# Kernel tuning notes

Measured on AMD Instinct MI355X. Metric: run time of the kernel, lower is better.

The kernel has to match this reference:

```python
import jax, jax.numpy as jnp
import numpy as np

B, D, O = 65536, 512, 64   # batch, input_size, output_size
E, T, K = 8, 2, 2          # num_experts, n_task, top-k
H1, H2 = 64, 32            # expert_hidden_layers (hardcoded in Expert)
LOSS_COEF = 0.01
EPS = 1e-10


def setup_inputs() -> dict:
    key = jax.random.key(0)
    ks = jax.random.split(key, 8)
    f32 = jnp.float32
    def rn(k, shape, scale):
        return jax.random.normal(k, shape, f32) * scale
    return {
        "x": jax.random.normal(ks[0], (B, D), f32),
        # gating params (one per task); init random so top-k routing is nontrivial
        "w_gates": rn(ks[1], (T, D, E), 0.02),
        "b_gates": jnp.zeros((T, E), f32),
        # per-expert MLP params, stacked over the expert axis
        "W1": rn(ks[2], (E, D, H1), 1.0 / np.sqrt(D)),
        "b1": jnp.zeros((E, H1), f32),
        "W2": rn(ks[3], (E, H1, H2), 1.0 / np.sqrt(H1)),
        "b2": jnp.zeros((E, H2), f32),
        "W3": rn(ks[4], (E, H2, O), 1.0 / np.sqrt(H2)),
        "b3": jnp.zeros((E, O), f32),
    }


def _cv_squared(v):
    # torch .var() default is unbiased (ddof=1)
    return jnp.var(v, ddof=1) / (jnp.mean(v) ** 2 + EPS)


def reference(x, w_gates, b_gates, W1, b1, W2, b2, W3, b3):
    # --- noisy_top_k_gating in eval mode (train=False): clean logits, top-k softmax ---
    logits = jnp.einsum("bd,tde->tbe", x, w_gates) + b_gates[:, None, :]  # [T,B,E]
    top_v, top_i = jax.lax.top_k(logits, K)                                # [T,B,K]
    top_g = jax.nn.softmax(top_v, axis=-1)                                 # [T,B,K]
    # scatter top-k gate values back to dense [T,B,E] (zeros elsewhere)
    gates = jnp.sum(jax.nn.one_hot(top_i, E, dtype=top_g.dtype) * top_g[..., None], axis=2)

    # --- experts: each token through each expert MLP (gates zero out non-selected,
    #     mathematically identical to dispatch/combine) ---
    h = jax.nn.relu(jnp.einsum("bd,edh->ebh", x, W1) + b1[:, None, :])     # [E,B,H1]
    h = jax.nn.relu(jnp.einsum("ebh,eho->ebo", h, W2) + b2[:, None, :])    # [E,B,H2]
    expert_out = jax.nn.relu(jnp.einsum("ebh,eho->ebo", h, W3) + b3[:, None, :])  # [E,B,O]

    # weighted combine per task
    y = jnp.einsum("tbe,ebo->tbo", gates, expert_out)                       # [T,B,O]

    # --- load balancing loss ---
    importance = gates.sum(axis=1)                          # [T,E]
    load = (gates > 0).sum(axis=1).astype(jnp.float32)      # [T,E]
    loss = LOSS_COEF * (jax.vmap(_cv_squared)(importance) + jax.vmap(_cv_squared)(load)).sum()
    return y, loss
```

## Files before the change

kernel.cpp:

```cpp
#include <hip/hip_runtime.h>


typedef short bfrag __attribute__((ext_vector_type(8)));
typedef float facc  __attribute__((ext_vector_type(4)));

#define MFMA16(a, b, c) __builtin_amdgcn_mfma_f32_16x16x32_bf16((a), (b), (c), 0, 0, 0)

__device__ __forceinline__ unsigned short bfbits(float f) {
  unsigned int u = __builtin_bit_cast(unsigned int, f);
  u += 0x7FFFu + ((u >> 16) & 1u);
  return (unsigned short)(u >> 16);
}
__device__ __forceinline__ unsigned pack2(float a, float b) {
  return (unsigned)bfbits(a) | ((unsigned)bfbits(b) << 16);
}
__device__ __forceinline__ float bf2f(unsigned short s) {
  unsigned int u = ((unsigned int)s) << 16;
  return __builtin_bit_cast(float, u);
}

#define G_OFF   65536
#define R_OFF   70656
#define A_OFF   72704
#define SM_SIZE 72832

__global__ __launch_bounds__(512, 4) void moe_fused(
    const float* __restrict__ x,
    const float* __restrict__ b_gates,
    const float* __restrict__ wgt,
    const float* __restrict__ b1,
    const float* __restrict__ b2,
    const float* __restrict__ b3,
    const bfrag* __restrict__ w1f,
    const bfrag* __restrict__ w2f,
    const bfrag* __restrict__ w3f,
    float* __restrict__ gacc_out,
    float* __restrict__ y)
{
  __shared__ alignas(16) char smem[SM_SIZE];
  const int tid = threadIdx.x;
  const int wave = tid >> 6, lane = tid & 63;
  const int q = lane & 15, g = lane >> 4;
  const int e = wave;
  const unsigned cb = (unsigned)e * 8192u;

  if (tid < 32) ((float*)(smem + A_OFF))[tid] = 0.f;

  const float* src = x + (size_t)blockIdx.x * 64 * 512 + lane * 512 + wave * 64;
  float4 fr[16];
  #pragma unroll
  for (int j = 0; j < 16; ++j) fr[j] = ((const float4*)src)[j];

  {
    int wu = __builtin_amdgcn_readfirstlane(wave);
    const float* wbase = wgt + wu * 64;
    float* pp = (float*)(smem + wave * 4096 + lane * 64);
    #pragma unroll
    for (int te = 0; te < 16; ++te) {
      const float* wrow = wbase + te * 512;
      float a0 = 0.f, a1 = 0.f, a2 = 0.f, a3 = 0.f;
      #pragma unroll
      for (int j = 0; j < 16; ++j) {
        a0 = fmaf(fr[j].x, wrow[j * 4 + 0], a0);
        a1 = fmaf(fr[j].y, wrow[j * 4 + 1], a1);
        a2 = fmaf(fr[j].z, wrow[j * 4 + 2], a2);
        a3 = fmaf(fr[j].w, wrow[j * 4 + 3], a3);
      }
      pp[(te + lane) & 15] = (a0 + a1) + (a2 + a3);
    }
  }
  __syncthreads();

  #pragma unroll
  for (int i0 = 0; i0 < 2; ++i0) {
    int i = i0 * 512 + tid;
    int tok = i >> 4, te = i & 15;
    const float* pb = (const float*)smem + tok * 16 + ((te + tok) & 15);
    float s = 0.f;
    #pragma unroll
    for (int w2 = 0; w2 < 8; ++w2) s += pb[w2 * 1024];
    ((float*)(smem + G_OFF))[tok * 20 + te] = s + b_gates[te];
  }
  __syncthreads();

  #pragma unroll
  for (int p = 0; p < 8; ++p) {
    uint4 v;
    v.x = pack2(fr[2 * p].x, fr[2 * p].y);
    v.y = pack2(fr[2 * p].z, fr[2 * p].w);
    v.z = pack2(fr[2 * p + 1].x, fr[2 * p + 1].y);
    v.w = pack2(fr[2 * p + 1].z, fr[2 * p + 1].w);
    unsigned byte = ((unsigned)(lane * 1024 + wave * 128 + p * 16)) ^ ((unsigned)(lane & 7) << 4);
    *(uint4*)(smem + byte) = v;
  }

  if (tid < 128) {
    int tok = tid >> 1, task = tid & 1;
    const float* Gr = (const float*)(smem + G_OFF) + tok * 20 + task * 8;
    float l[8];
    #pragma unroll
    for (int ee = 0; ee < 8; ++ee) l[ee] = Gr[ee];
    float v1 = l[0]; int e1 = 0;
    #pragma unroll
    for (int ee = 1; ee < 8; ++ee) { if (l[ee] > v1) { v1 = l[ee]; e1 = ee; } }
    float v2 = -3.4e38f; int e2 = 0;
    #pragma unroll
    for (int ee = 0; ee < 8; ++ee) {
      if (ee != e1 && l[ee] > v2) { v2 = l[ee]; e2 = ee; }
    }
    float g1 = 1.f / (1.f + __expf(v2 - v1));
    float g2 = 1.f - g1;
    float4 rec;
    rec.x = g1; rec.y = g2;
    rec.z = __int_as_float(e1); rec.w = __int_as_float(e2);
    ((float4*)(smem + R_OFF))[tok * 2 + task] = rec;
    float* lacc = (float*)(smem + A_OFF);
    atomicAdd(lacc + task * 8 + e1, g1);
    atomicAdd(lacc + task * 8 + e2, g2);
    atomicAdd(lacc + 16 + task * 8 + e1, 1.f);
    atomicAdd(lacc + 16 + task * 8 + e2, 1.f);
  }
  __syncthreads();

  facc acc[4][4];
  #pragma unroll
  for (int m = 0; m < 4; ++m)
    #pragma unroll
    for (int n = 0; n < 4; ++n) acc[m][n] = (facc)0.f;

  const bfrag* w1e = w1f + e * 4096 + lane;
  bfrag Bc[4], Bn[4];
  #pragma unroll
  for (int n = 0; n < 4; ++n) Bc[n] = w1e[n * 64];
  #pragma unroll
  for (int ks = 0; ks < 16; ++ks) {
    if (ks < 15) {
      #pragma unroll
      for (int n = 0; n < 4; ++n) Bn[n] = w1e[(ks + 1) * 256 + n * 64];
    }
    #pragma unroll
    for (int m = 0; m < 4; ++m) {
      unsigned ba = ((unsigned)((m * 16 + q) * 1024 + ks * 64 + g * 16)) ^ ((unsigned)(q & 7) << 4);
      bfrag A = *(const bfrag*)(smem + ba);
      #pragma unroll
      for (int n = 0; n < 4; ++n) acc[m][n] = MFMA16(A, Bc[n], acc[m][n]);
    }
    if (ks < 15) {
      #pragma unroll
      for (int n = 0; n < 4; ++n) Bc[n] = Bn[n];
    }
  }

  bfrag W2r[4];
  #pragma unroll
  for (int i = 0; i < 4; ++i) W2r[i] = w2f[e * 256 + i * 64 + lane];
  float b2v0 = b2[e * 32 + q];
  float b2v1 = b2[e * 32 + 16 + q];
  __syncthreads();

  {
    float bv[4];
    #pragma unroll
    for (int n = 0; n < 4; ++n) bv[n] = b1[e * 64 + n * 16 + q];
    #pragma unroll
    for (int m = 0; m < 4; ++m) {
      #pragma unroll
      for (int j = 0; j < 4; ++j) {
        float v0 = fmaxf(acc[m][0][j] + bv[0], 0.f);
        float v1 = fmaxf(acc[m][1][j] + bv[1], 0.f);
        float v2 = fmaxf(acc[m][2][j] + bv[2], 0.f);
        float v3 = fmaxf(acc[m][3][j] + bv[3], 0.f);
        int rr = m * 16 + g * 4 + j;
        unsigned byte = cb + (((unsigned)(rr * 128 + q * 8)) ^ ((unsigned)(rr & 7) << 4));
        uint2 p; p.x = pack2(v0, v1); p.y = pack2(v2, v3);
        *(uint2*)(smem + byte) = p;
      }
    }
  }

  {
    facc a2[4][2];
    #pragma unroll
    for (int m = 0; m < 4; ++m) { a2[m][0] = (facc)0.f; a2[m][1] = (facc)0.f; }
    #pragma unroll
    for (int ks = 0; ks < 2; ++ks) {
      #pragma unroll
      for (int m = 0; m < 4; ++m) {
        unsigned ba = cb + (((unsigned)((m * 16 + q) * 128 + ks * 64 + g * 16)) ^ ((unsigned)(q & 7) << 4));
        bfrag A = *(const bfrag*)(smem + ba);
        #pragma unroll
        for (int n = 0; n < 2; ++n) a2[m][n] = MFMA16(A, W2r[ks * 2 + n], a2[m][n]);
      }
    }
    bfrag W3r[4];
    #pragma unroll
    for (int n = 0; n < 4; ++n) W3r[n] = w3f[e * 256 + n * 64 + lane];
    float b3v[4];
    #pragma unroll
    for (int n = 0; n < 4; ++n) b3v[n] = b3[e * 64 + n * 16 + q];

    #pragma unroll
    for (int m = 0; m < 4; ++m) {
      #pragma unroll
      for (int j = 0; j < 4; ++j) {
        float v0 = fmaxf(a2[m][0][j] + b2v0, 0.f);
        float v1 = fmaxf(a2[m][1][j] + b2v1, 0.f);
        int rr = m * 16 + g * 4 + j;
        unsigned byte = cb + (((unsigned)(rr * 64 + q * 4)) ^ ((unsigned)(rr & 7) << 4));
        *(unsigned int*)(smem + byte) = pack2(v0, v1);
      }
    }

    facc a3[4][4];
    #pragma unroll
    for (int m = 0; m < 4; ++m)
      #pragma unroll
      for (int n = 0; n < 4; ++n) a3[m][n] = (facc)0.f;
    #pragma unroll
    for (int m = 0; m < 4; ++m) {
      unsigned ba = cb + (((unsigned)((m * 16 + q) * 64 + g * 16)) ^ ((unsigned)(q & 7) << 4));
      bfrag A = *(const bfrag*)(smem + ba);
      #pragma unroll
      for (int n = 0; n < 4; ++n) a3[m][n] = MFMA16(A, W3r[n], a3[m][n]);
    }
    #pragma unroll
    for (int m = 0; m < 4; ++m) {
      #pragma unroll
      for (int j = 0; j < 4; ++j) {
        float v0 = fmaxf(a3[m][0][j] + b3v[0], 0.f);
        float v1 = fmaxf(a3[m][1][j] + b3v[1], 0.f);
        float v2 = fmaxf(a3[m][2][j] + b3v[2], 0.f);
        float v3 = fmaxf(a3[m][3][j] + b3v[3], 0.f);
        int rr = m * 16 + g * 4 + j;
        unsigned byte = cb + (((unsigned)(rr * 128 + q * 8)) ^ ((unsigned)(rr & 7) << 4));
        uint2 p; p.x = pack2(v0, v1); p.y = pack2(v2, v3);
        *(uint2*)(smem + byte) = p;
      }
    }
  }
  __syncthreads();

  {
    int tsub = tid >> 4, u = tid & 15;
    const float4* recs = (const float4*)(smem + R_OFF);
    #pragma unroll
    for (int half = 0; half < 2; ++half) {
      int tok = tsub + half * 32;
      size_t trow = (size_t)blockIdx.x * 64 + tok;
      unsigned obyte = ((unsigned)(tok * 128 + u * 8)) ^ ((unsigned)(tok & 7) << 4);
      #pragma unroll
      for (int tt = 0; tt < 2; ++tt) {
        float4 rec = recs[tok * 2 + tt];
        float g1 = rec.x, g2 = rec.y;
        int e1 = __float_as_int(rec.z), e2 = __float_as_int(rec.w);
        uint2 o1 = *(const uint2*)(smem + e1 * 8192 + obyte);
        uint2 o2 = *(const uint2*)(smem + e2 * 8192 + obyte);
        unsigned short s1[4] = { (unsigned short)o1.x, (unsigned short)(o1.x >> 16),
                                 (unsigned short)o1.y, (unsigned short)(o1.y >> 16) };
        unsigned short s2[4] = { (unsigned short)o2.x, (unsigned short)(o2.x >> 16),
                                 (unsigned short)o2.y, (unsigned short)(o2.y >> 16) };
        float* yt = y + (size_t)tt * 4194304 + trow * 64;
        #pragma unroll
        for (int w = 0; w < 4; ++w) {
          yt[w * 16 + u] = g1 * bf2f(s1[w]) + g2 * bf2f(s2[w]);
        }
      }
    }
  }
  if (tid < 32) atomicAdd(gacc_out + tid, ((float*)(smem + A_OFF))[tid]);
  __syncthreads();

  if (tid == 0) {
    unsigned* cnt = (unsigned*)(gacc_out + 32);
    unsigned old = atomicAdd(cnt, 1u);
    if (old == gridDim.x - 1) {
      float loss = 0.f;
      #pragma unroll
      for (int a = 0; a < 4; ++a) {
        float v[8]; float mm = 0.f;
        #pragma unroll
        for (int i = 0; i < 8; ++i) {
          v[i] = __hip_atomic_load(gacc_out + a * 8 + i, __ATOMIC_RELAXED,
                                   __HIP_MEMORY_SCOPE_AGENT);
          mm += v[i];
        }
        mm *= 0.125f;
        float var = 0.f;
        #pragma unroll
        for (int i = 0; i < 8; ++i) { float d = v[i] - mm; var += d * d; }
        loss += (var * (1.f / 7.f)) / (mm * mm + 1e-10f);
      }
      y[8388608] = 0.01f * loss;
    }
  }
}

__global__ __launch_bounds__(256) void moe_prep(
    const float* __restrict__ W1, const float* __restrict__ W2,
    const float* __restrict__ W3, const float* __restrict__ wg,
    bfrag* __restrict__ w1f, bfrag* __restrict__ w2f,
    bfrag* __restrict__ w3f, float* __restrict__ wgt,
    float* __restrict__ gacc)
{
  int tid = blockIdx.x * 256 + threadIdx.x;
  bfrag o;
  if (tid < 32768) {
    int lane = tid & 63, nt = (tid >> 6) & 3, ks = (tid >> 8) & 15, e = tid >> 12;
    int q = lane & 15, g = lane >> 4;
    int hcol = nt * 16 + q;
    #pragma unroll
    for (int j = 0; j < 8; ++j) {
      int k = ks * 32 + g * 8 + j;
      o[j] = (short)bfbits(W1[((e * 512 + k) * 64) + hcol]);
    }
    w1f[tid] = o;
  } else if (tid < 34816) {
    int idx = tid - 32768;
    int lane = idx & 63, nt = (idx >> 6) & 1, ks = (idx >> 7) & 1, e = idx >> 8;
    int q = lane & 15, g = lane >> 4;
    int n = nt * 16 + q;
    #pragma unroll
    for (int j = 0; j < 8; ++j) {
      int s = ks * 32 + g * 8 + j;
      int hh = (s & 3) * 16 + (s >> 2);
      o[j] = (short)bfbits(W2[(e * 64 + hh) * 32 + n]);
    }
    w2f[idx] = o;
  } else if (tid < 36864) {
    int idx = tid - 34816;
    int lane = idx & 63, nt = (idx >> 6) & 3, e = idx >> 8;
    int q = lane & 15, g = lane >> 4;
    int ocol = nt * 16 + q;
    #pragma unroll
    for (int j = 0; j < 8; ++j) {
      int s = g * 8 + j;
      int hh = (s & 1) * 16 + (s >> 1);
      o[j] = (short)bfbits(W3[(e * 32 + hh) * 64 + ocol]);
    }
    w3f[idx] = o;
  } else if (tid < 45056) {
    int idx = tid - 36864;
    int te = idx >> 9, k = idx & 511;
    wgt[idx] = wg[(((te >> 3) * 512) + k) * 8 + (te & 7)];
  } else if (tid < 45089) {
    gacc[tid - 45056] = 0.f;
  }
}

extern "C" void kernel_launch(void* const* d_in, const int* in_sizes, int n_in,
                              void* d_out, int out_size, void* d_ws, size_t ws_size,
                              hipStream_t stream) {
  const float* x  = (const float*)d_in[0];
  const float* wg = (const float*)d_in[1];
  const float* bg = (const float*)d_in[2];
  const float* W1 = (const float*)d_in[3];
  const float* b1 = (const float*)d_in[4];
  const float* W2 = (const float*)d_in[5];
  const float* b2 = (const float*)d_in[6];
  const float* W3 = (const float*)d_in[7];
  const float* b3 = (const float*)d_in[8];
  float* y = (float*)d_out;

  char* ws = (char*)d_ws;
  float*  gacc = (float*)ws;
  bfrag*  w1f  = (bfrag*)(ws + 256);
  bfrag*  w2f  = (bfrag*)(ws + 524544);
  bfrag*  w3f  = (bfrag*)(ws + 557312);
  float*  wgt  = (float*)(ws + 590080);

  moe_prep<<<177, 256, 0, stream>>>(W1, W2, W3, wg, w1f, w2f, w3f, wgt, gacc);
  moe_fused<<<1024, 512, 0, stream>>>(x, bg, wgt, b1, b2, b3, w1f, w2f, w3f, gacc, y);
}
```

Before: 87.75 us.

## Halve tokens per block to 32 to cut LDS and registers for higher occupancy

Each block now processes 32 tokens instead of 64, with two lanes per token splitting the K range in the gating dot products. Shared memory roughly halves, per-wave accumulators shrink, and the grid doubles with launch bounds raised to 6 blocks per CU, all to raise occupancy and latency hiding. The W1 fragment double-buffer prefetch is removed. In exchange, W1, W2 and W3 fragments are re-read from global or L2 twice as often per token, the global atomics double, and the gate partial-sum reduction now spans 16 partials.

```diff
diff --git a/kernel.cpp b/kernel.cpp
--- a/kernel.cpp
+++ b/kernel.cpp
@@ -19,12 +19,12 @@
   return __builtin_bit_cast(float, u);
 }
 
-#define G_OFF   65536
-#define R_OFF   70656
-#define A_OFF   72704
-#define SM_SIZE 72832
-
-__global__ __launch_bounds__(512, 4) void moe_fused(
+#define G_OFF   32768
+#define R_OFF   34944
+#define A_OFF   35968
+#define SM_SIZE 36096
+
+__global__ __launch_bounds__(512, 6) void moe_fused(
     const float* __restrict__ x,
     const float* __restrict__ b_gates,
     const float* __restrict__ wgt,
@@ -42,61 +42,67 @@
   const int wave = tid >> 6, lane = tid & 63;
   const int q = lane & 15, g = lane >> 4;
   const int e = wave;
-  const unsigned cb = (unsigned)e * 8192u;
+  const unsigned cb = (unsigned)e * 4096u;
+  const int tok = lane & 31;
+  const int kh  = lane >> 5;
 
   if (tid < 32) ((float*)(smem + A_OFF))[tid] = 0.f;
 
-  const float* src = x + (size_t)blockIdx.x * 64 * 512 + lane * 512 + wave * 64;
-  float4 fr[16];
-  #pragma unroll
-  for (int j = 0; j < 16; ++j) fr[j] = ((const float4*)src)[j];
+  const float* src = x + (size_t)blockIdx.x * 32 * 512 + tok * 512 + wave * 64 + kh * 32;
+  float4 fr[8];
+  #pragma unroll
+  for (int j = 0; j < 8; ++j) fr[j] = ((const float4*)src)[j];
 
   {
     int wu = __builtin_amdgcn_readfirstlane(wave);
     const float* wbase = wgt + wu * 64;
-    float* pp = (float*)(smem + wave * 4096 + lane * 64);
+    float* pp = (float*)smem + ((wave * 2 + kh) * 32 + tok) * 16;
     #pragma unroll
     for (int te = 0; te < 16; ++te) {
       const float* wrow = wbase + te * 512;
       float a0 = 0.f, a1 = 0.f, a2 = 0.f, a3 = 0.f;
       #pragma unroll
-      for (int j = 0; j < 16; ++j) {
-        a0 = fmaf(fr[j].x, wrow[j * 4 + 0], a0);
-        a1 = fmaf(fr[j].y, wrow[j * 4 + 1], a1);
-        a2 = fmaf(fr[j].z, wrow[j * 4 + 2], a2);
-        a3 = fmaf(fr[j].w, wrow[j * 4 + 3], a3);
-      }
-      pp[(te + lane) & 15] = (a0 + a1) + (a2 + a3);
-    }
-  }
-  __syncthreads();
-
-  #pragma unroll
-  for (int i0 = 0; i0 < 2; ++i0) {
-    int i = i0 * 512 + tid;
-    int tok = i >> 4, te = i & 15;
-    const float* pb = (const float*)smem + tok * 16 + ((te + tok) & 15);
+      for (int j = 0; j < 8; ++j) {
+        float4 lo = *(const float4*)(wrow + j * 4);
+        float4 hi = *(const float4*)(wrow + 32 + j * 4);
+        float wx = kh ? hi.x : lo.x;
+        float wy = kh ? hi.y : lo.y;
+        float wz = kh ? hi.z : lo.z;
+        float ww = kh ? hi.w : lo.w;
+        a0 = fmaf(fr[j].x, wx, a0);
+        a1 = fmaf(fr[j].y, wy, a1);
+        a2 = fmaf(fr[j].z, wz, a2);
+        a3 = fmaf(fr[j].w, ww, a3);
+      }
+      pp[(te + (tok >> 1)) & 15] = (a0 + a1) + (a2 + a3);
+    }
+  }
+  __syncthreads();
+
+  {
+    int tk = tid >> 4, te = tid & 15;
+    const float* pb = (const float*)smem + tk * 16 + ((te + (tk >> 1)) & 15);
     float s = 0.f;
     #pragma unroll
-    for (int w2 = 0; w2 < 8; ++w2) s += pb[w2 * 1024];
-    ((float*)(smem + G_OFF))[tok * 20 + te] = s + b_gates[te];
-  }
-  __syncthreads();
-
-  #pragma unroll
-  for (int p = 0; p < 8; ++p) {
+    for (int c = 0; c < 16; ++c) s += pb[c * 512];
+    ((float*)(smem + G_OFF))[tk * 17 + te] = s + b_gates[te];
+  }
+  __syncthreads();
+
+  #pragma unroll
+  for (int p = 0; p < 4; ++p) {
     uint4 v;
     v.x = pack2(fr[2 * p].x, fr[2 * p].y);
     v.y = pack2(fr[2 * p].z, fr[2 * p].w);
     v.z = pack2(fr[2 * p + 1].x, fr[2 * p + 1].y);
     v.w = pack2(fr[2 * p + 1].z, fr[2 * p + 1].w);
-    unsigned byte = ((unsigned)(lane * 1024 + wave * 128 + p * 16)) ^ ((unsigned)(lane & 7) << 4);
+    unsigned byte = ((unsigned)(tok * 1024 + wave * 128 + kh * 64 + p * 16)) ^ ((unsigned)(tok & 7) << 4);
     *(uint4*)(smem + byte) = v;
   }
 
-  if (tid < 128) {
-    int tok = tid >> 1, task = tid & 1;
-    const float* Gr = (const float*)(smem + G_OFF) + tok * 20 + task * 8;
+  if (tid < 64) {
+    int ttok = tid >> 1, task = tid & 1;
+    const float* Gr = (const float*)(smem + G_OFF) + ttok * 17 + task * 8;
     float l[8];
     #pragma unroll
     for (int ee = 0; ee < 8; ++ee) l[ee] = Gr[ee];
@@ -113,7 +119,7 @@
     float4 rec;
     rec.x = g1; rec.y = g2;
     rec.z = __int_as_float(e1); rec.w = __int_as_float(e2);
-    ((float4*)(smem + R_OFF))[tok * 2 + task] = rec;
+    ((float4*)(smem + R_OFF))[ttok * 2 + task] = rec;
     float* lacc = (float*)(smem + A_OFF);
     atomicAdd(lacc + task * 8 + e1, g1);
     atomicAdd(lacc + task * 8 + e2, g2);
@@ -122,32 +128,27 @@
   }
   __syncthreads();
 
-  facc acc[4][4];
-  #pragma unroll
-  for (int m = 0; m < 4; ++m)
+  facc acc[2][4];
+  #pragma unroll
+  for (int m = 0; m < 2; ++m)
     #pragma unroll
     for (int n = 0; n < 4; ++n) acc[m][n] = (facc)0.f;
 
   const bfrag* w1e = w1f + e * 4096 + lane;
-  bfrag Bc[4], Bn[4];
-  #pragma unroll
-  for (int n = 0; n < 4; ++n) Bc[n] = w1e[n * 64];
   #pragma unroll
   for (int ks = 0; ks < 16; ++ks) {
-    if (ks < 15) {
-      #pragma unroll
-      for (int n = 0; n < 4; ++n) Bn[n] = w1e[(ks + 1) * 256 + n * 64];
-    }
-    #pragma unroll
-    for (int m = 0; m < 4; ++m) {
+    bfrag B0 = w1e[ks * 256];
+    bfrag B1 = w1e[ks * 256 + 64];
+    bfrag B2 = w1e[ks * 256 + 128];
+    bfrag B3 = w1e[ks * 256 + 192];
+    #pragma unroll
+    for (int m = 0; m < 2; ++m) {
       unsigned ba = ((unsigned)((m * 16 + q) * 1024 + ks * 64 + g * 16)) ^ ((unsigned)(q & 7) << 4);
       bfrag A = *(const bfrag*)(smem + ba);
-      #pragma unroll
-      for (int n = 0; n < 4; ++n) acc[m][n] = MFMA16(A, Bc[n], acc[m][n]);
-    }
-    if (ks < 15) {
-      #pragma unroll
-      for (int n = 0; n < 4; ++n) Bc[n] = Bn[n];
+      acc[m][0] = MFMA16(A, B0, acc[m][0]);
+      acc[m][1] = MFMA16(A, B1, acc[m][1]);
+      acc[m][2] = MFMA16(A, B2, acc[m][2]);
+      acc[m][3] = MFMA16(A, B3, acc[m][3]);
     }
   }
 
@@ -163,7 +164,7 @@
     #pragma unroll
     for (int n = 0; n < 4; ++n) bv[n] = b1[e * 64 + n * 16 + q];
     #pragma unroll
-    for (int m = 0; m < 4; ++m) {
+    for (int m = 0; m < 2; ++m) {
       #pragma unroll
       for (int j = 0; j < 4; ++j) {
         float v0 = fmaxf(acc[m][0][j] + bv[0], 0.f);
@@ -172,24 +173,24 @@
         float v3 = fmaxf(acc[m][3][j] + bv[3], 0.f);
         int rr = m * 16 + g * 4 + j;
         unsigned byte = cb + (((unsigned)(rr * 128 + q * 8)) ^ ((unsigned)(rr & 7) << 4));
-        uint2 p; p.x = pack2(v0, v1); p.y = pack2(v2, v3);
-        *(uint2*)(smem + byte) = p;
-      }
-    }
-  }
-
-  {
-    facc a2[4][2];
-    #pragma unroll
-    for (int m = 0; m < 4; ++m) { a2[m][0] = (facc)0.f; a2[m][1] = (facc)0.f; }
+        uint2 pk; pk.x = pack2(v0, v1); pk.y = pack2(v2, v3);
+        *(uint2*)(smem + byte) = pk;
+      }
+    }
+  }
+
+  {
+    facc a2[2][2];
+    #pragma unroll
+    for (int m = 0; m < 2; ++m) { a2[m][0] = (facc)0.f; a2[m][1] = (facc)0.f; }
     #pragma unroll
     for (int ks = 0; ks < 2; ++ks) {
       #pragma unroll
-      for (int m = 0; m < 4; ++m) {
+      for (int m = 0; m < 2; ++m) {
         unsigned ba = cb + (((unsigned)((m * 16 + q) * 128 + ks * 64 + g * 16)) ^ ((unsigned)(q & 7) << 4));
         bfrag A = *(const bfrag*)(smem + ba);
-        #pragma unroll
-        for (int n = 0; n < 2; ++n) a2[m][n] = MFMA16(A, W2r[ks * 2 + n], a2[m][n]);
+        a2[m][0] = MFMA16(A, W2r[ks * 2], a2[m][0]);
+        a2[m][1] = MFMA16(A, W2r[ks * 2 + 1], a2[m][1]);
       }
     }
     bfrag W3r[4];
@@ -200,7 +201,7 @@
     for (int n = 0; n < 4; ++n) b3v[n] = b3[e * 64 + n * 16 + q];
 
     #pragma unroll
-    for (int m = 0; m < 4; ++m) {
+    for (int m = 0; m < 2; ++m) {
       #pragma unroll
       for (int j = 0; j < 4; ++j) {
         float v0 = fmaxf(a2[m][0][j] + b2v0, 0.f);
@@ -211,20 +212,20 @@
       }
     }
 
-    facc a3[4][4];
-    #pragma unroll
-    for (int m = 0; m < 4; ++m)
+    facc a3[2][4];
+    #pragma unroll
+    for (int m = 0; m < 2; ++m)
       #pragma unroll
       for (int n = 0; n < 4; ++n) a3[m][n] = (facc)0.f;
     #pragma unroll
-    for (int m = 0; m < 4; ++m) {
+    for (int m = 0; m < 2; ++m) {
       unsigned ba = cb + (((unsigned)((m * 16 + q) * 64 + g * 16)) ^ ((unsigned)(q & 7) << 4));
       bfrag A = *(const bfrag*)(smem + ba);
       #pragma unroll
       for (int n = 0; n < 4; ++n) a3[m][n] = MFMA16(A, W3r[n], a3[m][n]);
     }
     #pragma unroll
-    for (int m = 0; m < 4; ++m) {
+    for (int m = 0; m < 2; ++m) {
       #pragma unroll
       for (int j = 0; j < 4; ++j) {
         float v0 = fmaxf(a3[m][0][j] + b3v[0], 0.f);
@@ -233,37 +234,33 @@
         float v3 = fmaxf(a3[m][3][j] + b3v[3], 0.f);
         int rr = m * 16 + g * 4 + j;
         unsigned byte = cb + (((unsigned)(rr * 128 + q * 8)) ^ ((unsigned)(rr & 7) << 4));
-        uint2 p; p.x = pack2(v0, v1); p.y = pack2(v2, v3);
-        *(uint2*)(smem + byte) = p;
-      }
-    }
-  }
-  __syncthreads();
-
-  {
-    int tsub = tid >> 4, u = tid & 15;
+        uint2 pk; pk.x = pack2(v0, v1); pk.y = pack2(v2, v3);
+        *(uint2*)(smem + byte) = pk;
+      }
+    }
+  }
+  __syncthreads();
+
+  {
+    int ct = tid >> 4, u = tid & 15;
+    size_t trow = (size_t)blockIdx.x * 32 + ct;
+    unsigned obyte = ((unsigned)(ct * 128 + u * 8)) ^ ((unsigned)(ct & 7) << 4);
     const float4* recs = (const float4*)(smem + R_OFF);
     #pragma unroll
-    for (int half = 0; half < 2; ++half) {
-      int tok = tsub + half * 32;
-      size_t trow = (size_t)blockIdx.x * 64 + tok;
-      unsigned obyte = ((unsigned)(tok * 128 + u * 8)) ^ ((unsigned)(tok & 7) << 4);
-      #pragma unroll
-      for (int tt = 0; tt < 2; ++tt) {
-        float4 rec = recs[tok * 2 + tt];
-        float g1 = rec.x, g2 = rec.y;
-        int e1 = __float_as_int(rec.z), e2 = __float_as_int(rec.w);
-        uint2 o1 = *(const uint2*)(smem + e1 * 8192 + obyte);
-        uint2 o2 = *(const uint2*)(smem + e2 * 8192 + obyte);
-        unsigned short s1[4] = { (unsigned short)o1.x, (unsigned short)(o1.x >> 16),
-                                 (unsigned short)o1.y, (unsigned short)(o1.y >> 16) };
-        unsigned short s2[4] = { (unsigned short)o2.x, (unsigned short)(o2.x >> 16),
-                                 (unsigned short)o2.y, (unsigned short)(o2.y >> 16) };
-        float* yt = y + (size_t)tt * 4194304 + trow * 64;
-        #pragma unroll
-        for (int w = 0; w < 4; ++w) {
-          yt[w * 16 + u] = g1 * bf2f(s1[w]) + g2 * bf2f(s2[w]);
-        }
+    for (int tt = 0; tt < 2; ++tt) {
+      float4 rec = recs[ct * 2 + tt];
+      float g1 = rec.x, g2 = rec.y;
+      int e1 = __float_as_int(rec.z), e2 = __float_as_int(rec.w);
+      uint2 o1 = *(const uint2*)(smem + e1 * 4096 + obyte);
+      uint2 o2 = *(const uint2*)(smem + e2 * 4096 + obyte);
+      unsigned short s1[4] = { (unsigned short)o1.x, (unsigned short)(o1.x >> 16),
+                               (unsigned short)o1.y, (unsigned short)(o1.y >> 16) };
+      unsigned short s2[4] = { (unsigned short)o2.x, (unsigned short)(o2.x >> 16),
+                               (unsigned short)o2.y, (unsigned short)(o2.y >> 16) };
+      float* yt = y + (size_t)tt * 4194304 + trow * 64;
+      #pragma unroll
+      for (int w = 0; w < 4; ++w) {
+        yt[w * 16 + u] = g1 * bf2f(s1[w]) + g2 * bf2f(s2[w]);
       }
     }
   }
@@ -369,5 +366,5 @@
   float*  wgt  = (float*)(ws + 590080);
 
   moe_prep<<<177, 256, 0, stream>>>(W1, W2, W3, wg, w1f, w2f, w3f, wgt, gacc);
-  moe_fused<<<1024, 512, 0, stream>>>(x, bg, wgt, b1, b2, b3, w1f, w2f, w3f, gacc, y);
-}
+  moe_fused<<<2048, 512, 0, stream>>>(x, bg, wgt, b1, b2, b3, w1f, w2f, w3f, gacc, y);
+}
```

New measurement: 132.8 us. +51.3%, slower.
